# Kernel optimization log

Hardware: AMD Instinct MI355X
Metric: run time of the kernel (lower is better)

The kernel has to match this reference:

```python
import jax, jax.numpy as jnp
import numpy as np


def _cheb_conv(x, row, col, norm, W, b, num_nodes):
    # PyG ChebConv with sym normalization and lambda_max=2:
    # L_hat = -D^{-1/2} A D^{-1/2} (off-diagonal), diagonal exactly 0.
    # Tx_0 = x; Tx_1 = L_hat x; Tx_k = 2 L_hat Tx_{k-1} - Tx_{k-2}
    K = W.shape[0]
    Tx0 = x
    out = Tx0 @ W[0]
    Tx1 = jax.ops.segment_sum(norm[:, None] * Tx0[col], row, num_segments=num_nodes)
    out = out + Tx1 @ W[1]
    for k in range(2, K):
        Tx2 = 2.0 * jax.ops.segment_sum(norm[:, None] * Tx1[col], row, num_segments=num_nodes) - Tx0
        out = out + Tx2 @ W[k]
        Tx0, Tx1 = Tx1, Tx2
    return out + b


def setup_inputs() -> dict:
    key = jax.random.key(0)
    ks = jax.random.split(key, 8)
    N, E, D, H, C, K = 100000, 1600000, 128, 64, 5, 3
    x = jax.random.normal(ks[0], (N, D), dtype=jnp.float32)
    edge_index = jax.random.randint(ks[1], (2, E), 0, N, dtype=jnp.int64)
    edge_weight = jax.random.uniform(ks[2], (E,), dtype=jnp.float32)
    s1 = 1.0 / np.sqrt(D)
    s3 = 1.0 / np.sqrt(H)
    W1 = jax.random.normal(ks[3], (K, D, H), dtype=jnp.float32) * s1
    W3 = jax.random.normal(ks[4], (K, H, H), dtype=jnp.float32) * s3
    W4 = jax.random.normal(ks[5], (K, H, C), dtype=jnp.float32) * s3
    return {
        "x": x, "edge_index": edge_index, "edge_weight": edge_weight,
        "W1": W1, "b1": jnp.zeros((H,), jnp.float32),
        "W3": W3, "b3": jnp.zeros((H,), jnp.float32),
        "W4": W4, "b4": jnp.zeros((C,), jnp.float32),
    }


def reference(x, edge_index, edge_weight, W1, b1, W3, b3, W4, b4):
    N = x.shape[0]
    row, col = edge_index[0], edge_index[1]
    # symmetric normalization of the scaled Laplacian (lambda_max = 2)
    deg = jax.ops.segment_sum(edge_weight, row, num_segments=N)
    dinv = jnp.where(deg > 0, jax.lax.rsqrt(jnp.where(deg > 0, deg, 1.0)), 0.0)
    norm = -dinv[row] * edge_weight * dinv[col]
    # dropout is a no-op in eval mode (training=False)
    h = jax.nn.relu(_cheb_conv(x, row, col, norm, W1, b1, N))
    h = jax.nn.relu(_cheb_conv(h, row, col, norm, W3, b3, N))
    h = _cheb_conv(h, row, col, norm, W4, b4, N)
    return jax.nn.log_softmax(h, axis=1)
```

## Files before the change

kernel.cpp:

```cpp
#include <hip/hip_runtime.h>
#include <cstdint>
#include <cstddef>

typedef unsigned short u16;
typedef __attribute__((ext_vector_type(8))) short bf16x8;
typedef __attribute__((ext_vector_type(4))) float f32x4;

#define PB 1024
#define MAXB 1024

__device__ __forceinline__ float bflo(unsigned u) { return __uint_as_float(u << 16); }
__device__ __forceinline__ float bfhi(unsigned u) { return __uint_as_float(u & 0xFFFF0000u); }
__device__ __forceinline__ u16 f2bf(float f) {
    unsigned u = __float_as_uint(f);
    u += 0x7FFFu + ((u >> 16) & 1u);
    return (u16)(u >> 16);
}
__device__ __forceinline__ unsigned pack2(float a, float b) {
    return (unsigned)f2bf(a) | ((unsigned)f2bf(b) << 16);
}


__global__ __launch_bounds__(256) void binA(const int* __restrict__ row, int* __restrict__ P,
                                            int E, int NB, int EB) {
    __shared__ int hist[MAXB];
    int b = blockIdx.x;
    for (int i = threadIdx.x; i < NB; i += 256) hist[i] = 0;
    __syncthreads();
    int e0 = b * EB, e1 = min(E, e0 + EB);
    for (int e = e0 + threadIdx.x; e < e1; e += 256)
        atomicAdd(&hist[row[e] >> 7], 1);
    __syncthreads();
    for (int i = threadIdx.x; i < NB; i += 256) P[(size_t)i * PB + b] = hist[i];
}

__global__ __launch_bounds__(256) void binB1(int* __restrict__ P, int* __restrict__ bintot) {
    __shared__ int sh[256];
    int* p = P + (size_t)blockIdx.x * PB;
    int tid = threadIdx.x;
    int base = tid * 4;
    int v[4];
#pragma unroll
    for (int j = 0; j < 4; ++j) v[j] = p[base + j];
    int s = v[0] + v[1] + v[2] + v[3];
    sh[tid] = s;
    __syncthreads();
    for (int off = 1; off < 256; off <<= 1) {
        int t = (tid >= off) ? sh[tid - off] : 0;
        __syncthreads();
        sh[tid] += t;
        __syncthreads();
    }
    int run = sh[tid] - s;
#pragma unroll
    for (int j = 0; j < 4; ++j) { p[base + j] = run; run += v[j]; }
    if (tid == 255) bintot[blockIdx.x] = sh[255];
}

__global__ __launch_bounds__(256) void binB2(const int* __restrict__ bintot,
                                             int* __restrict__ bstart, int NB) {
    __shared__ int sh[256];
    int tid = threadIdx.x;
    int base = tid * 4;
    int v[4];
#pragma unroll
    for (int j = 0; j < 4; ++j) v[j] = (base + j < NB) ? bintot[base + j] : 0;
    int s = v[0] + v[1] + v[2] + v[3];
    sh[tid] = s;
    __syncthreads();
    for (int off = 1; off < 256; off <<= 1) {
        int t = (tid >= off) ? sh[tid - off] : 0;
        __syncthreads();
        sh[tid] += t;
        __syncthreads();
    }
    int run = sh[tid] - s;
#pragma unroll
    for (int j = 0; j < 4; ++j) {
        if (base + j < NB) bstart[base + j] = run;
        run += v[j];
    }
    if (tid == 255) bstart[NB] = sh[255];
}

__global__ __launch_bounds__(256) void binC(const int* __restrict__ row, const int* __restrict__ col,
                                            const float* __restrict__ w, const int* __restrict__ P,
                                            const int* __restrict__ bstart, int2* __restrict__ rec,
                                            int E, int NB, int EB) {
    __shared__ int cur[MAXB];
    int b = blockIdx.x;
    for (int i = threadIdx.x; i < NB; i += 256)
        cur[i] = bstart[i] + P[(size_t)i * PB + b];
    __syncthreads();
    int e0 = b * EB, e1 = min(E, e0 + EB);
    for (int e = e0 + threadIdx.x; e < e1; e += 256) {
        int r = row[e];
        int bin = r >> 7;
        int slot = atomicAdd(&cur[bin], 1);
        rec[slot] = make_int2(col[e] | ((r & 127) << 17), __float_as_int(w[e]));
    }
}

__global__ __launch_bounds__(256) void binD(const int2* __restrict__ rec,
                                            const int* __restrict__ bstart,
                                            int2* __restrict__ meta, int* __restrict__ rowp,
                                            float* __restrict__ dinv, int N, int NB) {
    __shared__ int cnt[128], st[128], cur[128];
    __shared__ float deg[128];
    int bin = blockIdx.x;
    int tid = threadIdx.x;
    if (tid < 128) { cnt[tid] = 0; deg[tid] = 0.f; }
    __syncthreads();
    int e0 = bstart[bin], e1 = bstart[bin + 1];
    for (int e = e0 + tid; e < e1; e += 256) {
        int2 v = rec[e];
        int rl = (v.x >> 17) & 127;
        atomicAdd(&cnt[rl], 1);
        atomicAdd(&deg[rl], __int_as_float(v.y));
    }
    __syncthreads();
    if (tid < 128) st[tid] = cnt[tid];
    __syncthreads();
    for (int off = 1; off < 128; off <<= 1) {
        int t = (tid >= off && tid < 128) ? st[tid - off] : 0;
        __syncthreads();
        if (tid < 128) st[tid] += t;
        __syncthreads();
    }
    int rows = min(128, N - bin * 128);
    if (tid < 128) {
        int excl = st[tid] - cnt[tid];
        cur[tid] = e0 + excl;
        if (tid < rows) {
            rowp[bin * 128 + tid] = e0 + excl;
            float d = deg[tid];
            dinv[bin * 128 + tid] = d > 0.f ? rsqrtf(d) : 0.f;
        }
    }
    if (bin == NB - 1 && tid == 0) rowp[N] = e1;
    __syncthreads();
    for (int e = e0 + tid; e < e1; e += 256) {
        int2 v = rec[e];
        int rl = (v.x >> 17) & 127;
        int slot = atomicAdd(&cur[rl], 1);
        meta[slot] = make_int2(v.x & 0x1FFFF, v.y);
    }
}

__global__ void scale_ev(const int* __restrict__ rowp, int2* __restrict__ meta,
                         const float* __restrict__ dinv, int n) {
    int r = blockIdx.x * blockDim.x + threadIdx.x;
    if (r >= n) return;
    int e0 = rowp[r], e1 = rowp[r + 1];
    float dr = dinv[r];
    int e = e0;
    for (; e + 4 <= e1; e += 4) {
        int2 v0 = meta[e], v1 = meta[e + 1], v2 = meta[e + 2], v3 = meta[e + 3];
        float d0 = dinv[v0.x], d1 = dinv[v1.x], d2 = dinv[v2.x], d3 = dinv[v3.x];
        v0.y = __float_as_int(-dr * __int_as_float(v0.y) * d0);
        v1.y = __float_as_int(-dr * __int_as_float(v1.y) * d1);
        v2.y = __float_as_int(-dr * __int_as_float(v2.y) * d2);
        v3.y = __float_as_int(-dr * __int_as_float(v3.y) * d3);
        meta[e] = v0; meta[e + 1] = v1; meta[e + 2] = v2; meta[e + 3] = v3;
    }
    for (; e < e1; ++e) {
        int2 v = meta[e];
        v.y = __float_as_int(-dr * __int_as_float(v.y) * dinv[v.x]);
        meta[e] = v;
    }
}

__global__ void to_bf16(const float* __restrict__ in, unsigned* __restrict__ out, int n2) {
    int i = blockIdx.x * blockDim.x + threadIdx.x;
    if (i < n2) {
        float2 v = reinterpret_cast<const float2*>(in)[i];
        out[i] = pack2(v.x, v.y);
    }
}

__global__ void wpack_all(const float* __restrict__ W1, const float* __restrict__ W3,
                          const float* __restrict__ W4, u16* __restrict__ Wpu,
                          u16* __restrict__ Wp3, u16* __restrict__ Wpp) {
    int gi = blockIdx.x * blockDim.x + threadIdx.x;
    if (gi < 3072) {
        int idx = gi;
        int lane = idx & 63;
        int nt = (idx >> 6) % 12;
        int kt = idx / 768;
        int krow = kt * 32 + (lane >> 4) * 8;
        int c = nt * 16 + (lane & 15);
        u16 tmp[8];
#pragma unroll
        for (int j = 0; j < 8; ++j) {
            int k = krow + j;
            float v;
            if (c < 64)       v = W1[(size_t)k * 64 + c] - W1[2 * 8192 + (size_t)k * 64 + c];
            else if (c < 128) v = W1[8192 + (size_t)k * 64 + (c - 64)];
            else              v = W1[2 * 8192 + (size_t)k * 64 + (c - 128)];
            tmp[j] = f2bf(v);
        }
        *reinterpret_cast<uint4*>(Wpu + (size_t)idx * 8) = *reinterpret_cast<const uint4*>(tmp);
    } else if (gi < 3072 + 1536) {
        int idx = gi - 3072;
        int lane = idx & 63;
        int nt = (idx >> 6) & 3;
        int kt = idx >> 8;
        int krow = kt * 32 + (lane >> 4) * 8;
        int c = nt * 16 + (lane & 15);
        u16 tmp[8];
#pragma unroll
        for (int j = 0; j < 8; ++j) tmp[j] = f2bf(W3[(size_t)(krow + j) * 64 + c]);
        *reinterpret_cast<uint4*>(Wp3 + (size_t)idx * 8) = *reinterpret_cast<const uint4*>(tmp);
    } else if (gi < 3072 + 1536 + 256) {
        int idx = gi - (3072 + 1536);
        int lane = idx & 63;
        int nt = (idx >> 6) & 1;
        int kt = idx >> 7;
        int krow = kt * 32 + (lane >> 4) * 8;
        int c = nt * 16 + (lane & 15);
        u16 tmp[8];
#pragma unroll
        for (int j = 0; j < 8; ++j) {
            int k = krow + j;
            float v = 0.f;
            if (c < 5)                  v = W4[(size_t)k * 5 + c] - W4[640 + (size_t)k * 5 + c];
            else if (c >= 8 && c < 13)  v = W4[320 + (size_t)k * 5 + (c - 8)];
            else if (c >= 16 && c < 21) v = W4[640 + (size_t)k * 5 + (c - 16)];
            tmp[j] = f2bf(v);
        }
        *reinterpret_cast<uint4*>(Wpp + (size_t)idx * 8) = *reinterpret_cast<const uint4*>(tmp);
    }
}

template <int MODE>
__global__ __launch_bounds__(256) void spmm64(const int* __restrict__ rp,
                                              const int2* __restrict__ meta,
                                              const u16* __restrict__ x,
                                              const u16* __restrict__ z,
                                              const float* __restrict__ bias,
                                              u16* __restrict__ y, int n) {
    int r = blockIdx.x * 32 + (threadIdx.x >> 3);
    if (r >= n) return;
    int f = (threadIdx.x & 7) * 8;
    int e0 = rp[r], e1 = rp[r + 1];
    float acc[8] = {0.f, 0.f, 0.f, 0.f, 0.f, 0.f, 0.f, 0.f};
    auto fma8 = [&](uint4 xv, float w) {
        acc[0] += w * bflo(xv.x); acc[1] += w * bfhi(xv.x);
        acc[2] += w * bflo(xv.y); acc[3] += w * bfhi(xv.y);
        acc[4] += w * bflo(xv.z); acc[5] += w * bfhi(xv.z);
        acc[6] += w * bflo(xv.w); acc[7] += w * bfhi(xv.w);
    };
    int e = e0;
    for (; e + 4 <= e1; e += 4) {
        int2 m0 = meta[e], m1 = meta[e + 1], m2 = meta[e + 2], m3 = meta[e + 3];
        uint4 v0 = *reinterpret_cast<const uint4*>(x + (size_t)m0.x * 64 + f);
        uint4 v1 = *reinterpret_cast<const uint4*>(x + (size_t)m1.x * 64 + f);
        uint4 v2 = *reinterpret_cast<const uint4*>(x + (size_t)m2.x * 64 + f);
        uint4 v3 = *reinterpret_cast<const uint4*>(x + (size_t)m3.x * 64 + f);
        fma8(v0, __int_as_float(m0.y));
        fma8(v1, __int_as_float(m1.y));
        fma8(v2, __int_as_float(m2.y));
        fma8(v3, __int_as_float(m3.y));
    }
    for (; e < e1; ++e) {
        int2 m = meta[e];
        uint4 xv = *reinterpret_cast<const uint4*>(x + (size_t)m.x * 64 + f);
        fma8(xv, __int_as_float(m.y));
    }
    if (MODE == 1 || MODE == 2) {
        uint4 zv = *reinterpret_cast<const uint4*>(z + (size_t)r * 64 + f);
        float zz[8] = {bflo(zv.x), bfhi(zv.x), bflo(zv.y), bfhi(zv.y),
                       bflo(zv.z), bfhi(zv.z), bflo(zv.w), bfhi(zv.w)};
#pragma unroll
        for (int j = 0; j < 8; ++j)
            acc[j] = (MODE == 1) ? 2.f * acc[j] + zz[j] : 2.f * acc[j] - zz[j];
    } else if (MODE == 3) {
        uint4 zv = *reinterpret_cast<const uint4*>(z + (size_t)r * 64 + f);
        float zz[8] = {bflo(zv.x), bfhi(zv.x), bflo(zv.y), bfhi(zv.y),
                       bflo(zv.z), bfhi(zv.z), bflo(zv.w), bfhi(zv.w)};
        float4 bl = *reinterpret_cast<const float4*>(bias + f);
        float4 bh = *reinterpret_cast<const float4*>(bias + f + 4);
        float bb[8] = {bl.x, bl.y, bl.z, bl.w, bh.x, bh.y, bh.z, bh.w};
#pragma unroll
        for (int j = 0; j < 8; ++j) acc[j] = fmaxf(acc[j] + zz[j] + bb[j], 0.f);
    }
    uint4 o;
    o.x = pack2(acc[0], acc[1]);
    o.y = pack2(acc[2], acc[3]);
    o.z = pack2(acc[4], acc[5]);
    o.w = pack2(acc[6], acc[7]);
    *reinterpret_cast<uint4*>(y + (size_t)r * 64 + f) = o;
}

__device__ __forceinline__ void spmm8_acc(const int* rp, const int2* meta, const u16* x,
                                          int r, int t, float* acc) {
    int e0 = rp[r], e1 = rp[r + 1];
    auto fma8 = [&](uint4 xv, float w) {
        acc[0] += w * bflo(xv.x); acc[1] += w * bfhi(xv.x);
        acc[2] += w * bflo(xv.y); acc[3] += w * bfhi(xv.y);
        acc[4] += w * bflo(xv.z); acc[5] += w * bfhi(xv.z);
        acc[6] += w * bflo(xv.w); acc[7] += w * bfhi(xv.w);
    };
    int e = e0 + t;
    for (; e + 4 < e1; e += 8) {
        int2 m0 = meta[e], m1 = meta[e + 4];
        uint4 v0 = *reinterpret_cast<const uint4*>(x + (size_t)m0.x * 8);
        uint4 v1 = *reinterpret_cast<const uint4*>(x + (size_t)m1.x * 8);
        fma8(v0, __int_as_float(m0.y));
        fma8(v1, __int_as_float(m1.y));
    }
    for (; e < e1; e += 4) {
        int2 m = meta[e];
        uint4 xv = *reinterpret_cast<const uint4*>(x + (size_t)m.x * 8);
        fma8(xv, __int_as_float(m.y));
    }
#pragma unroll
    for (int j = 0; j < 8; ++j) acc[j] += __shfl_xor(acc[j], 1);
#pragma unroll
    for (int j = 0; j < 8; ++j) acc[j] += __shfl_xor(acc[j], 2);
}

__global__ __launch_bounds__(256) void spmm8_p2(const int* __restrict__ rp,
                                                const int2* __restrict__ meta,
                                                const u16* __restrict__ x,
                                                const u16* __restrict__ z,
                                                u16* __restrict__ y, int n) {
    int r = blockIdx.x * 64 + (threadIdx.x >> 2);
    if (r >= n) return;
    int t = threadIdx.x & 3;
    float acc[8] = {0.f, 0.f, 0.f, 0.f, 0.f, 0.f, 0.f, 0.f};
    spmm8_acc(rp, meta, x, r, t, acc);
    if (t == 0) {
        uint4 zv = *reinterpret_cast<const uint4*>(z + (size_t)r * 8);
        float zz[8] = {bflo(zv.x), bfhi(zv.x), bflo(zv.y), bfhi(zv.y),
                       bflo(zv.z), bfhi(zv.z), bflo(zv.w), bfhi(zv.w)};
        uint4 o;
        o.x = pack2(2.f * acc[0] + zz[0], 2.f * acc[1] + zz[1]);
        o.y = pack2(2.f * acc[2] + zz[2], 2.f * acc[3] + zz[3]);
        o.z = pack2(2.f * acc[4] + zz[4], 2.f * acc[5] + zz[5]);
        o.w = pack2(2.f * acc[6] + zz[6], 2.f * acc[7] + zz[7]);
        *reinterpret_cast<uint4*>(y + (size_t)r * 8) = o;
    }
}

__global__ __launch_bounds__(256) void spmm8_lsm(const int* __restrict__ rp,
                                                 const int2* __restrict__ meta,
                                                 const u16* __restrict__ x,
                                                 const u16* __restrict__ z,
                                                 const float* __restrict__ bias,
                                                 float* __restrict__ out, int n) {
    int r = blockIdx.x * 64 + (threadIdx.x >> 2);
    if (r >= n) return;
    int t = threadIdx.x & 3;
    float acc[8] = {0.f, 0.f, 0.f, 0.f, 0.f, 0.f, 0.f, 0.f};
    spmm8_acc(rp, meta, x, r, t, acc);
    if (t == 0) {
        uint4 zv = *reinterpret_cast<const uint4*>(z + (size_t)r * 8);
        float zz[8] = {bflo(zv.x), bfhi(zv.x), bflo(zv.y), bfhi(zv.y),
                       bflo(zv.z), bfhi(zv.z), bflo(zv.w), bfhi(zv.w)};
        float val[5];
#pragma unroll
        for (int j = 0; j < 5; ++j) val[j] = acc[j] + zz[j] + bias[j];
        float mx = val[0];
#pragma unroll
        for (int j = 1; j < 5; ++j) mx = fmaxf(mx, val[j]);
        float s = 0.f;
#pragma unroll
        for (int j = 0; j < 5; ++j) s += expf(val[j] - mx);
        float l = logf(s);
#pragma unroll
        for (int j = 0; j < 5; ++j) out[(size_t)r * 5 + j] = val[j] - mx - l;
    }
}


__global__ __launch_bounds__(256) void gemm_u(const u16* __restrict__ A,
                                              const u16* __restrict__ Wp,
                                              u16* __restrict__ u0, u16* __restrict__ u1,
                                              u16* __restrict__ u2, int n) {
    int wave = threadIdx.x >> 6;
    int lane = threadIdx.x & 63;
    int r0 = blockIdx.x * 64 + wave * 16;
    int row = r0 + (lane & 15);
    int rowc = row < n ? row : n - 1;
    int kofs = (lane >> 4) * 8;
    f32x4 acc[12] = {};
    for (int kt = 0; kt < 4; ++kt) {
        bf16x8 a = *reinterpret_cast<const bf16x8*>(A + (size_t)rowc * 128 + kt * 32 + kofs);
        const u16* wb = Wp + (size_t)kt * 12 * 512 + (size_t)lane * 8;
#pragma unroll
        for (int nt = 0; nt < 12; ++nt) {
            bf16x8 b = *reinterpret_cast<const bf16x8*>(wb + nt * 512);
            acc[nt] = __builtin_amdgcn_mfma_f32_16x16x32_bf16(a, b, acc[nt], 0, 0, 0);
        }
    }
    int col = lane & 15;
    u16* U[3] = {u0, u1, u2};
#pragma unroll
    for (int nt = 0; nt < 12; ++nt) {
        u16* dst = U[nt >> 2];
        int cc = (nt & 3) * 16 + col;
#pragma unroll
        for (int i = 0; i < 4; ++i) {
            int rr = r0 + (lane >> 4) * 4 + i;
            if (rr < n) dst[(size_t)rr * 64 + cc] = f2bf(acc[nt][i]);
        }
    }
}

__global__ __launch_bounds__(256) void gemm3_mfma(const u16* __restrict__ A0,
                                                  const u16* __restrict__ A1,
                                                  const u16* __restrict__ A2,
                                                  const u16* __restrict__ Wp,
                                                  const float* __restrict__ bias,
                                                  u16* __restrict__ out, int n) {
    int wave = threadIdx.x >> 6;
    int lane = threadIdx.x & 63;
    int r0 = blockIdx.x * 64 + wave * 16;
    int row = r0 + (lane & 15);
    int rowc = row < n ? row : n - 1;
    int kofs = (lane >> 4) * 8;
    const u16* Ap[3] = {A0, A1, A2};
    f32x4 acc[4] = {};
    for (int kt = 0; kt < 6; ++kt) {
        const u16* Asrc = Ap[kt >> 1];
        int c0 = (kt & 1) * 32;
        bf16x8 a = *reinterpret_cast<const bf16x8*>(Asrc + (size_t)rowc * 64 + c0 + kofs);
        const u16* wb = Wp + (size_t)kt * 4 * 512 + (size_t)lane * 8;
#pragma unroll
        for (int nt = 0; nt < 4; ++nt) {
            bf16x8 b = *reinterpret_cast<const bf16x8*>(wb + nt * 512);
            acc[nt] = __builtin_amdgcn_mfma_f32_16x16x32_bf16(a, b, acc[nt], 0, 0, 0);
        }
    }
    int col = lane & 15;
#pragma unroll
    for (int nt = 0; nt < 4; ++nt) {
        float bb = bias[nt * 16 + col];
#pragma unroll
        for (int i = 0; i < 4; ++i) {
            int rr = r0 + (lane >> 4) * 4 + i;
            if (rr < n) {
                float v = fmaxf(acc[nt][i] + bb, 0.f);
                out[(size_t)rr * 64 + nt * 16 + col] = f2bf(v);
            }
        }
    }
}

__global__ __launch_bounds__(256) void gemm_proj(const u16* __restrict__ A,
                                                 const u16* __restrict__ Wp,
                                                 u16* __restrict__ p0, u16* __restrict__ p1,
                                                 u16* __restrict__ p2, int n) {
    int wave = threadIdx.x >> 6;
    int lane = threadIdx.x & 63;
    int r0 = blockIdx.x * 64 + wave * 16;
    int row = r0 + (lane & 15);
    int rowc = row < n ? row : n - 1;
    int kofs = (lane >> 4) * 8;
    f32x4 acc[2] = {};
    for (int kt = 0; kt < 2; ++kt) {
        bf16x8 a = *reinterpret_cast<const bf16x8*>(A + (size_t)rowc * 64 + kt * 32 + kofs);
        const u16* wb = Wp + (size_t)kt * 2 * 512 + (size_t)lane * 8;
#pragma unroll
        for (int nt = 0; nt < 2; ++nt) {
            bf16x8 b = *reinterpret_cast<const bf16x8*>(wb + nt * 512);
            acc[nt] = __builtin_amdgcn_mfma_f32_16x16x32_bf16(a, b, acc[nt], 0, 0, 0);
        }
    }
    int col = lane & 15;
    u16* P[3] = {p0, p1, p2};
#pragma unroll
    for (int nt = 0; nt < 2; ++nt) {
        int c = nt * 16 + col;
        if (c < 24) {
            u16* dst = P[c >> 3];
            int j = c & 7;
#pragma unroll
            for (int i = 0; i < 4; ++i) {
                int rr = r0 + (lane >> 4) * 4 + i;
                if (rr < n) dst[(size_t)rr * 8 + j] = f2bf(acc[nt][i]);
            }
        }
    }
}


static inline size_t alignup(size_t v) { return (v + 255) & ~(size_t)255; }

extern "C" void kernel_launch(void* const* d_in, const int* in_sizes, int n_in,
                              void* d_out, int out_size, void* d_ws, size_t ws_size,
                              hipStream_t stream) {
    const float* x  = (const float*)d_in[0];
    const int*   ei = (const int*)d_in[1];
    const float* ew = (const float*)d_in[2];
    const float* W1 = (const float*)d_in[3];
    const float* b1 = (const float*)d_in[4];
    const float* W3 = (const float*)d_in[5];
    const float* b3 = (const float*)d_in[6];
    const float* W4 = (const float*)d_in[7];
    const float* b4 = (const float*)d_in[8];
    float* out = (float*)d_out;

    const int D = 128, H = 64;
    const int N = in_sizes[0] / D;
    const int E = in_sizes[2];
    const int* row = ei;
    const int* col = ei + E;

    char* ws = (char*)d_ws;
    size_t off = 0;
    auto alloc = [&](size_t bytes) { size_t o = off; off += alignup(bytes); return o; };

    float* dinv   = (float*)(ws + alloc((size_t)N * 4));
    int*   rowp   = (int*)  (ws + alloc((size_t)(N + 1) * 4));
    int*   bintot = (int*)  (ws + alloc(MAXB * 4));
    int*   bstart = (int*)  (ws + alloc((MAXB + 1) * 4));
    int*   P      = (int*)  (ws + alloc((size_t)MAXB * PB * 4));
    int2*  meta   = (int2*) (ws + alloc((size_t)E * 8));
    int2*  rec    = (int2*) (ws + alloc((size_t)E * 8));
    u16*   xb     = (u16*)  (ws + alloc((size_t)N * D * 2));
    u16*   A      = (u16*)  (ws + alloc((size_t)N * H * 2));
    u16*   B      = (u16*)  (ws + alloc((size_t)N * H * 2));
    u16*   C      = (u16*)  (ws + alloc((size_t)N * H * 2));
    u16*   Dd     = (u16*)  (ws + alloc((size_t)N * H * 2));
    u16*   P0     = (u16*)  (ws + alloc((size_t)N * 8 * 2));
    u16*   P1     = (u16*)  (ws + alloc((size_t)N * 8 * 2));
    u16*   P2     = (u16*)  (ws + alloc((size_t)N * 8 * 2));
    u16*   P3     = (u16*)  (ws + alloc((size_t)N * 8 * 2));
    u16*   Wpu    = (u16*)  (ws + alloc((size_t)4 * 12 * 512 * 2));
    u16*   Wp3    = (u16*)  (ws + alloc((size_t)6 * 4 * 512 * 2));
    u16*   Wpp    = (u16*)  (ws + alloc((size_t)2 * 2 * 512 * 2));

    const int NB = (N + 127) >> 7;
    const int EB = (E + PB - 1) / PB;

    dim3 blk(256);
    int gN = (N + 255) / 256;

    binA<<<PB, blk, 0, stream>>>(row, P, E, NB, EB);
    binB1<<<NB, blk, 0, stream>>>(P, bintot);
    binB2<<<1, blk, 0, stream>>>(bintot, bstart, NB);
    binC<<<PB, blk, 0, stream>>>(row, col, ew, P, bstart, rec, E, NB, EB);
    binD<<<NB, blk, 0, stream>>>(rec, bstart, meta, rowp, dinv, N, NB);
    scale_ev<<<gN, blk, 0, stream>>>(rowp, meta, dinv, N);

    int n2 = N * D / 2;
    to_bf16<<<(n2 + 255) / 256, blk, 0, stream>>>(x, (unsigned*)xb, n2);
    wpack_all<<<(4864 + 255) / 256, blk, 0, stream>>>(W1, W3, W4, Wpu, Wp3, Wpp);

    int g64 = (N + 31) / 32;
    int gG  = (N + 63) / 64;
    int g8  = (N + 63) / 64;

    gemm_u<<<gG, blk, 0, stream>>>(xb, Wpu, A, B, C, N);
    spmm64<1><<<g64, blk, 0, stream>>>(rowp, meta, C, B, nullptr, Dd, N);
    spmm64<3><<<g64, blk, 0, stream>>>(rowp, meta, Dd, A, b1, B, N);

    spmm64<0><<<g64, blk, 0, stream>>>(rowp, meta, B, nullptr, nullptr, C, N);
    spmm64<2><<<g64, blk, 0, stream>>>(rowp, meta, C, B, nullptr, A, N);
    gemm3_mfma<<<gG, blk, 0, stream>>>(B, C, A, Wp3, b3, Dd, N);

    gemm_proj<<<gG, blk, 0, stream>>>(Dd, Wpp, P0, P1, P2, N);
    spmm8_p2<<<g8, blk, 0, stream>>>(rowp, meta, P2, P1, P3, N);
    spmm8_lsm<<<g8, blk, 0, stream>>>(rowp, meta, P3, P0, b4, out, N);
}
```

Baseline: 306.3 us.

## Use coarser 1024-row bins for CSR build and merge small kernels

Row bins for the two-level counting sort grow from 128 to 1024 rows, so there are about 98 bins instead of 782. The bin-start prefix scan is recomputed inside binC and binD, which removes the separate binB2 launch. The to_bf16 and weight-pack kernels are merged into a single prep launch. The aim is fewer launches and smaller histogram traffic, at the cost of 1024-thread binD blocks with far fewer blocks in flight and more shared-memory atomic contention per bin.

```diff
diff --git a/kernel.cpp b/kernel.cpp
--- a/kernel.cpp
+++ b/kernel.cpp
@@ -7,7 +7,7 @@
 typedef __attribute__((ext_vector_type(4))) float f32x4;
 
 #define PB 1024
-#define MAXB 1024
+#define MAXSB 128
 
 __device__ __forceinline__ float bflo(unsigned u) { return __uint_as_float(u << 16); }
 __device__ __forceinline__ float bfhi(unsigned u) { return __uint_as_float(u & 0xFFFF0000u); }
@@ -23,15 +23,15 @@
 
 __global__ __launch_bounds__(256) void binA(const int* __restrict__ row, int* __restrict__ P,
                                             int E, int NB, int EB) {
-    __shared__ int hist[MAXB];
+    __shared__ int hist[MAXSB];
     int b = blockIdx.x;
-    for (int i = threadIdx.x; i < NB; i += 256) hist[i] = 0;
+    if (threadIdx.x < MAXSB) hist[threadIdx.x] = 0;
     __syncthreads();
     int e0 = b * EB, e1 = min(E, e0 + EB);
     for (int e = e0 + threadIdx.x; e < e1; e += 256)
-        atomicAdd(&hist[row[e] >> 7], 1);
-    __syncthreads();
-    for (int i = threadIdx.x; i < NB; i += 256) P[(size_t)i * PB + b] = hist[i];
+        atomicAdd(&hist[row[e] >> 10], 1);
+    __syncthreads();
+    if (threadIdx.x < NB) P[(size_t)threadIdx.x * PB + b] = hist[threadIdx.x];
 }
 
 __global__ __launch_bounds__(256) void binB1(int* __restrict__ P, int* __restrict__ bintot) {
@@ -57,91 +57,83 @@
     if (tid == 255) bintot[blockIdx.x] = sh[255];
 }
 
-__global__ __launch_bounds__(256) void binB2(const int* __restrict__ bintot,
-                                             int* __restrict__ bstart, int NB) {
-    __shared__ int sh[256];
-    int tid = threadIdx.x;
-    int base = tid * 4;
-    int v[4];
-#pragma unroll
-    for (int j = 0; j < 4; ++j) v[j] = (base + j < NB) ? bintot[base + j] : 0;
-    int s = v[0] + v[1] + v[2] + v[3];
-    sh[tid] = s;
-    __syncthreads();
-    for (int off = 1; off < 256; off <<= 1) {
-        int t = (tid >= off) ? sh[tid - off] : 0;
-        __syncthreads();
-        sh[tid] += t;
-        __syncthreads();
-    }
-    int run = sh[tid] - s;
-#pragma unroll
-    for (int j = 0; j < 4; ++j) {
-        if (base + j < NB) bstart[base + j] = run;
-        run += v[j];
-    }
-    if (tid == 255) bstart[NB] = sh[255];
-}
-
 __global__ __launch_bounds__(256) void binC(const int* __restrict__ row, const int* __restrict__ col,
                                             const float* __restrict__ w, const int* __restrict__ P,
-                                            const int* __restrict__ bstart, int2* __restrict__ rec,
+                                            const int* __restrict__ bintot, int2* __restrict__ rec,
                                             int E, int NB, int EB) {
-    __shared__ int cur[MAXB];
+    __shared__ int bs[MAXSB];
+    __shared__ int cur[MAXSB];
     int b = blockIdx.x;
-    for (int i = threadIdx.x; i < NB; i += 256)
-        cur[i] = bstart[i] + P[(size_t)i * PB + b];
+    int tid = threadIdx.x;
+    if (tid < MAXSB) bs[tid] = (tid < NB) ? bintot[tid] : 0;
+    __syncthreads();
+    for (int off = 1; off < MAXSB; off <<= 1) {
+        int t = (tid >= off && tid < MAXSB) ? bs[tid - off] : 0;
+        __syncthreads();
+        if (tid < MAXSB) bs[tid] += t;
+        __syncthreads();
+    }
+    if (tid < NB) cur[tid] = (tid ? bs[tid - 1] : 0) + P[(size_t)tid * PB + b];
     __syncthreads();
     int e0 = b * EB, e1 = min(E, e0 + EB);
-    for (int e = e0 + threadIdx.x; e < e1; e += 256) {
+    for (int e = e0 + tid; e < e1; e += 256) {
         int r = row[e];
-        int bin = r >> 7;
+        int bin = r >> 10;
         int slot = atomicAdd(&cur[bin], 1);
-        rec[slot] = make_int2(col[e] | ((r & 127) << 17), __float_as_int(w[e]));
-    }
-}
-
-__global__ __launch_bounds__(256) void binD(const int2* __restrict__ rec,
-                                            const int* __restrict__ bstart,
-                                            int2* __restrict__ meta, int* __restrict__ rowp,
-                                            float* __restrict__ dinv, int N, int NB) {
-    __shared__ int cnt[128], st[128], cur[128];
-    __shared__ float deg[128];
+        rec[slot] = make_int2(col[e] | ((r & 1023) << 17), __float_as_int(w[e]));
+    }
+}
+
+__global__ __launch_bounds__(1024) void binD(const int2* __restrict__ rec,
+                                             const int* __restrict__ bintot,
+                                             int2* __restrict__ meta, int* __restrict__ rowp,
+                                             float* __restrict__ dinv, int N, int NB) {
+    __shared__ int bs[MAXSB];
+    __shared__ int cnt[1024], st[1024], cur[1024];
+    __shared__ float deg[1024];
     int bin = blockIdx.x;
     int tid = threadIdx.x;
-    if (tid < 128) { cnt[tid] = 0; deg[tid] = 0.f; }
-    __syncthreads();
-    int e0 = bstart[bin], e1 = bstart[bin + 1];
-    for (int e = e0 + tid; e < e1; e += 256) {
+    if (tid < MAXSB) bs[tid] = (tid < NB) ? bintot[tid] : 0;
+    cnt[tid] = 0;
+    deg[tid] = 0.f;
+    __syncthreads();
+    for (int off = 1; off < MAXSB; off <<= 1) {
+        int t = (tid >= off && tid < MAXSB) ? bs[tid - off] : 0;
+        __syncthreads();
+        if (tid < MAXSB) bs[tid] += t;
+        __syncthreads();
+    }
+    int e0 = bin ? bs[bin - 1] : 0;
+    int e1 = bs[bin];
+    __syncthreads();
+    for (int e = e0 + tid; e < e1; e += 1024) {
         int2 v = rec[e];
-        int rl = (v.x >> 17) & 127;
+        int rl = (v.x >> 17) & 1023;
         atomicAdd(&cnt[rl], 1);
         atomicAdd(&deg[rl], __int_as_float(v.y));
     }
     __syncthreads();
-    if (tid < 128) st[tid] = cnt[tid];
-    __syncthreads();
-    for (int off = 1; off < 128; off <<= 1) {
-        int t = (tid >= off && tid < 128) ? st[tid - off] : 0;
-        __syncthreads();
-        if (tid < 128) st[tid] += t;
-        __syncthreads();
-    }
-    int rows = min(128, N - bin * 128);
-    if (tid < 128) {
-        int excl = st[tid] - cnt[tid];
-        cur[tid] = e0 + excl;
-        if (tid < rows) {
-            rowp[bin * 128 + tid] = e0 + excl;
-            float d = deg[tid];
-            dinv[bin * 128 + tid] = d > 0.f ? rsqrtf(d) : 0.f;
-        }
+    st[tid] = cnt[tid];
+    __syncthreads();
+    for (int off = 1; off < 1024; off <<= 1) {
+        int t = (tid >= off) ? st[tid - off] : 0;
+        __syncthreads();
+        st[tid] += t;
+        __syncthreads();
+    }
+    int rows = min(1024, N - bin * 1024);
+    int excl = st[tid] - cnt[tid];
+    cur[tid] = e0 + excl;
+    if (tid < rows) {
+        rowp[bin * 1024 + tid] = e0 + excl;
+        float d = deg[tid];
+        dinv[bin * 1024 + tid] = d > 0.f ? rsqrtf(d) : 0.f;
     }
     if (bin == NB - 1 && tid == 0) rowp[N] = e1;
     __syncthreads();
-    for (int e = e0 + tid; e < e1; e += 256) {
+    for (int e = e0 + tid; e < e1; e += 1024) {
         int2 v = rec[e];
-        int rl = (v.x >> 17) & 127;
+        int rl = (v.x >> 17) & 1023;
         int slot = atomicAdd(&cur[rl], 1);
         meta[slot] = make_int2(v.x & 0x1FFFF, v.y);
     }
@@ -170,17 +162,10 @@
     }
 }
 
-__global__ void to_bf16(const float* __restrict__ in, unsigned* __restrict__ out, int n2) {
-    int i = blockIdx.x * blockDim.x + threadIdx.x;
-    if (i < n2) {
-        float2 v = reinterpret_cast<const float2*>(in)[i];
-        out[i] = pack2(v.x, v.y);
-    }
-}
-
-__global__ void wpack_all(const float* __restrict__ W1, const float* __restrict__ W3,
-                          const float* __restrict__ W4, u16* __restrict__ Wpu,
-                          u16* __restrict__ Wp3, u16* __restrict__ Wpp) {
+__global__ void prep(const float* __restrict__ x, unsigned* __restrict__ xb, int n2,
+                     const float* __restrict__ W1, const float* __restrict__ W3,
+                     const float* __restrict__ W4, u16* __restrict__ Wpu,
+                     u16* __restrict__ Wp3, u16* __restrict__ Wpp) {
     int gi = blockIdx.x * blockDim.x + threadIdx.x;
     if (gi < 3072) {
         int idx = gi;
@@ -229,6 +214,12 @@
             tmp[j] = f2bf(v);
         }
         *reinterpret_cast<uint4*>(Wpp + (size_t)idx * 8) = *reinterpret_cast<const uint4*>(tmp);
+    } else {
+        int i = gi - 4864;
+        if (i < n2) {
+            float2 v = reinterpret_cast<const float2*>(x)[i];
+            xb[i] = pack2(v.x, v.y);
+        }
     }
 }
 
@@ -514,9 +505,8 @@
 
     float* dinv   = (float*)(ws + alloc((size_t)N * 4));
     int*   rowp   = (int*)  (ws + alloc((size_t)(N + 1) * 4));
-    int*   bintot = (int*)  (ws + alloc(MAXB * 4));
-    int*   bstart = (int*)  (ws + alloc((MAXB + 1) * 4));
-    int*   P      = (int*)  (ws + alloc((size_t)MAXB * PB * 4));
+    int*   bintot = (int*)  (ws + alloc(MAXSB * 4));
+    int*   P      = (int*)  (ws + alloc((size_t)MAXSB * PB * 4));
     int2*  meta   = (int2*) (ws + alloc((size_t)E * 8));
     int2*  rec    = (int2*) (ws + alloc((size_t)E * 8));
     u16*   xb     = (u16*)  (ws + alloc((size_t)N * D * 2));
@@ -532,7 +522,7 @@
     u16*   Wp3    = (u16*)  (ws + alloc((size_t)6 * 4 * 512 * 2));
     u16*   Wpp    = (u16*)  (ws + alloc((size_t)2 * 2 * 512 * 2));
 
-    const int NB = (N + 127) >> 7;
+    const int NB = (N + 1023) >> 10;
     const int EB = (E + PB - 1) / PB;
 
     dim3 blk(256);
@@ -540,14 +530,13 @@
 
     binA<<<PB, blk, 0, stream>>>(row, P, E, NB, EB);
     binB1<<<NB, blk, 0, stream>>>(P, bintot);
-    binB2<<<1, blk, 0, stream>>>(bintot, bstart, NB);
-    binC<<<PB, blk, 0, stream>>>(row, col, ew, P, bstart, rec, E, NB, EB);
-    binD<<<NB, blk, 0, stream>>>(rec, bstart, meta, rowp, dinv, N, NB);
+    binC<<<PB, blk, 0, stream>>>(row, col, ew, P, bintot, rec, E, NB, EB);
+    binD<<<NB, dim3(1024), 0, stream>>>(rec, bintot, meta, rowp, dinv, N, NB);
     scale_ev<<<gN, blk, 0, stream>>>(rowp, meta, dinv, N);
 
     int n2 = N * D / 2;
-    to_bf16<<<(n2 + 255) / 256, blk, 0, stream>>>(x, (unsigned*)xb, n2);
-    wpack_all<<<(4864 + 255) / 256, blk, 0, stream>>>(W1, W3, W4, Wpu, Wp3, Wpp);
+    prep<<<(n2 + 4864 + 255) / 256, blk, 0, stream>>>(x, (unsigned*)xb, n2, W1, W3, W4,
+                                                      Wpu, Wp3, Wpp);
 
     int g64 = (N + 31) / 32;
     int gG  = (N + 63) / 64;
```

Measured after the change: 308.5 us. About the same (+0.7%).
